# Kernel tuning notes

Hardware: AMD Instinct MI355X
Metric: run time of the kernel (lower is better)

## Reference

```python
import jax, jax.numpy as jnp
import numpy as np

K = 5  # up_kernel

def bilinear(x, hw):
    # torch F.interpolate bilinear, align_corners=False (half-pixel), no antialias
    return jax.image.resize(x, x.shape[:2] + hw, method='linear', antialias=False)

def nearest2x(x):
    return jnp.repeat(jnp.repeat(x, 2, axis=2), 2, axis=3)

def conv3x3(x, w, b):
    y = jax.lax.conv_general_dilated(x, w, (1, 1), [(1, 1), (1, 1)],
                                     dimension_numbers=('NCHW', 'OIHW', 'NCHW'))
    return y + b[None, :, None, None]

def carafe(x, mask):
    # x: [N,C,H,W]; mask: [N,K*K,H,W] softmax-normalized. scale_factor=1, up_group=1.
    N, C, H, W = x.shape
    r = K // 2
    xp = jnp.pad(x, ((0, 0), (0, 0), (r, r), (r, r)))
    out = jnp.zeros_like(x)
    idx = 0
    for di in range(K):
        for dj in range(K):
            out = out + xp[:, :, di:di + H, dj:dj + W] * mask[:, idx:idx + 1]
            idx += 1
    return out

def setup_inputs() -> dict:
    key = jax.random.key(0)
    ks = jax.random.split(key, 6)
    feat = jax.random.normal(ks[0], (1, 32, 96, 96), jnp.float32)
    seg = jax.random.normal(ks[1], (1, 19, 96, 96), jnp.float32)
    img = jax.random.uniform(ks[2], (1, 3, 384, 384), jnp.float32)
    w_enc0 = jax.random.normal(ks[3], (25, 35, 3, 3), jnp.float32) * 0.05
    b_enc0 = jnp.zeros((25,), jnp.float32)
    w_enc1 = jax.random.normal(ks[4], (25, 35, 3, 3), jnp.float32) * 0.05
    b_enc1 = jnp.zeros((25,), jnp.float32)
    return {'feat': feat, 'seg': seg, 'img': img,
            'w_enc0': w_enc0, 'b_enc0': b_enc0, 'w_enc1': w_enc1, 'b_enc1': b_enc1}

def reference(feat, seg, img, w_enc0, b_enc0, w_enc1, b_enc1):
    weights = [(w_enc0, b_enc0), (w_enc1, b_enc1)]
    for i in range(2):
        Hf, Wf = feat.shape[-2], feat.shape[-1]
        resized_img = bilinear(img, (2 * Hf, 2 * Wf))
        # high-boost filtering: img_hf = img - lowpass(img) + img
        lr = bilinear(resized_img, (Hf, Wf))
        lr = bilinear(lr, (2 * Hf, 2 * Wf))
        img_hf = 2.0 * resized_img - lr
        feat_up = nearest2x(feat)
        seg_up = nearest2x(seg)
        w, b = weights[i]
        mask = conv3x3(jnp.concatenate([feat_up, img_hf], axis=1), w, b)
        # kernel_normalizer: pixel_shuffle(1)=identity, softmax over the 25 kernel taps
        mask = jax.nn.softmax(mask, axis=1)
        seg = carafe(seg_up, mask)
        feat = carafe(feat_up, mask)
    return seg
```

## Files before the change

kernel.cpp:

```cpp
#include <hip/hip_runtime.h>


#define TPB 256

__global__ __launch_bounds__(TPB) void repack_kernel(
    const float* __restrict__ w, float* __restrict__ W2, float* __restrict__ wTh) {
  int i = blockIdx.x * TPB + threadIdx.x;
  if (i < 12800) {
    int oc = i % 25; int j = i / 25;
    int src = j & 3; j >>= 2;
    int ic = j & 31; int p = j >> 5;
    int py = p >> 1, px = p & 1;
    int a = src >> 1, b = src & 1;
    float s = 0.f;
    for (int ky = 0; ky < 3; ++ky) {
      int rs = (py == 0) ? (ky >= 1) : (ky >= 2);
      if (rs != a) continue;
      for (int kx = 0; kx < 3; ++kx) {
        int cs = (px == 0) ? (kx >= 1) : (kx >= 2);
        if (cs != b) continue;
        s += w[oc * 315 + ic * 9 + ky * 3 + kx];
      }
    }
    W2[i] = s;
  } else if (i < 12800 + 675) {
    int k = i - 12800;
    int oc = k % 25; int j = k / 25;
    int h = j % 3; int tap = j / 3;
    wTh[k] = w[oc * 315 + (32 + h) * 9 + tap];
  }
}

__global__ __launch_bounds__(TPB) void down2_kernel(
    const float* __restrict__ in, float* __restrict__ out, int C, int H, int W) {
  int idx = blockIdx.x * blockDim.x + threadIdx.x;
  int N = C * H * W;
  if (idx >= N) return;
  int x = idx % W; int t = idx / W; int y = t % H; int c = t / H;
  const float* p = in + ((c * 2 * H) + 2 * y) * (2 * W) + 2 * x;
  out[idx] = 0.25f * (p[0] + p[1] + p[2 * W] + p[2 * W + 1]);
}

__global__ __launch_bounds__(TPB) void highboost_kernel(
    const float* __restrict__ base, const float* __restrict__ lr,
    float* __restrict__ out, int C, int H, int W) {
  const int OH = 2 * H, OW = 2 * W;
  int idx = blockIdx.x * blockDim.x + threadIdx.x;
  int N = C * OH * OW;
  if (idx >= N) return;
  int x = idx % OW; int t = idx / OW; int y = t % OH; int c = t / OH;
  int m = y >> 1; int ya, yb; float wya, wyb;
  if ((y & 1) == 0) { ya = (m - 1 < 0) ? 0 : m - 1; yb = m; wya = 0.25f; wyb = 0.75f; }
  else             { ya = m; yb = (m + 1 >= H) ? H - 1 : m + 1; wya = 0.75f; wyb = 0.25f; }
  int n = x >> 1; int xa, xb; float wxa, wxb;
  if ((x & 1) == 0) { xa = (n - 1 < 0) ? 0 : n - 1; xb = n; wxa = 0.25f; wxb = 0.75f; }
  else             { xa = n; xb = (n + 1 >= W) ? W - 1 : n + 1; wxa = 0.75f; wxb = 0.25f; }
  const float* p = lr + c * H * W;
  float up = wya * (wxa * p[ya * W + xa] + wxb * p[ya * W + xb])
           + wyb * (wxa * p[yb * W + xa] + wxb * p[yb * W + xb]);
  out[idx] = 2.0f * base[idx] - up;
}

__global__ __launch_bounds__(512, 4) void conv_softmax_kernel(
    const float* __restrict__ feat, const float* __restrict__ hf,
    const float* __restrict__ W2, const float* __restrict__ wTh,
    const float* __restrict__ b, float* __restrict__ mask,
    int Hf, int Wf) {
  const int OH = 2 * Hf, OW = 2 * Wf, Np = OH * OW, fplane = Hf * Wf;
  __shared__ float red[8][64][26];

  const int t = threadIdx.x;
  const int lane = t & 63;
  const int s = __builtin_amdgcn_readfirstlane(t >> 6);
  const int par = blockIdx.x & 3;
  const int bt = blockIdx.x >> 2;
  const int TW = Wf >> 5;
  const int gx0 = (bt % TW) << 5;
  const int gy0 = (bt / TW) << 1;
  const int py = par >> 1, px = par & 1;
  const int gy = gy0 + (lane >> 5);
  const int gx = gx0 + (lane & 31);

  int r0 = gy - 1 + py; const bool zr0 = (r0 < 0);      if (zr0) r0 = 0;
  int r1 = gy + py;     const bool zr1 = (r1 >= Hf);    if (zr1) r1 = Hf - 1;
  int c0 = gx - 1 + px; const bool zc0 = (c0 < 0);      if (zc0) c0 = 0;
  int c1 = gx + px;     const bool zc1 = (c1 >= Wf);    if (zc1) c1 = Wf - 1;
  const int o00 = r0 * Wf + c0, o01 = r0 * Wf + c1;
  const int o10 = r1 * Wf + c0, o11 = r1 * Wf + c1;

  float acc[25];
#pragma unroll
  for (int oc = 0; oc < 25; ++oc) acc[oc] = 0.f;

  const int fbeg_tab[8] = {0, 3, 6, 9, 14, 19, 24, 28};
  const int fend_tab[8] = {3, 6, 9, 14, 19, 24, 28, 32};
  const int fbeg = fbeg_tab[s], fend = fend_tab[s];

  for (int ic = fbeg; ic < fend; ++ic) {
    const float* fp = feat + ic * fplane;
    float v00 = (zr0 | zc0) ? 0.f : fp[o00];
    float v01 = (zr0 | zc1) ? 0.f : fp[o01];
    float v10 = (zr1 | zc0) ? 0.f : fp[o10];
    float v11 = (zr1 | zc1) ? 0.f : fp[o11];
    const float* wp = W2 + (size_t)((par * 32 + ic) * 4) * 25;
#pragma unroll
    for (int oc = 0; oc < 25; ++oc)
      acc[oc] += v00 * wp[oc] + v01 * wp[25 + oc] + v10 * wp[50 + oc] + v11 * wp[75 + oc];
  }

  if (s < 3) {
    const int x = 2 * gx + px, y = 2 * gy + py;
    const float* hp = hf + s * Np;
#pragma unroll
    for (int ky = 0; ky < 3; ++ky) {
      int yy = y + ky - 1;
      bool vy = (yy >= 0) && (yy < OH);
      int yo = (vy ? yy : 0) * OW;
#pragma unroll
      for (int kx = 0; kx < 3; ++kx) {
        int xx = x + kx - 1;
        bool vv = vy && (xx >= 0) && (xx < OW);
        float v = vv ? hp[yo + (vv ? xx : 0)] : 0.f;
        const float* wp = wTh + ((ky * 3 + kx) * 3 + s) * 25;
#pragma unroll
        for (int oc = 0; oc < 25; ++oc) acc[oc] = fmaf(v, wp[oc], acc[oc]);
      }
    }
  }

#pragma unroll
  for (int oc = 0; oc < 25; ++oc) red[s][lane][oc] = acc[oc];
  __syncthreads();
  for (int i = t; i < 1600; i += 512) {
    int oc = i % 25, p2 = i / 25;
    float sum = red[0][p2][oc];
#pragma unroll
    for (int k = 1; k < 8; ++k) sum += red[k][p2][oc];
    red[0][p2][oc] = sum + b[oc];
  }
  __syncthreads();
  if (t < 64) {
    float mx = red[0][t][0];
#pragma unroll
    for (int oc = 1; oc < 25; ++oc) mx = fmaxf(mx, red[0][t][oc]);
    float ssum = 0.f;
#pragma unroll
    for (int oc = 0; oc < 25; ++oc) {
      float e = __expf(red[0][t][oc] - mx); red[0][t][oc] = e; ssum += e;
    }
    float inv = 1.0f / ssum;
#pragma unroll
    for (int oc = 0; oc < 25; ++oc) red[0][t][oc] *= inv;
  }
  __syncthreads();
  {
    const int p2 = t & 63;
    const int gy2 = gy0 + (p2 >> 5), gx2 = gx0 + (p2 & 31);
    const int pix = (2 * gy2 + py) * OW + (2 * gx2 + px);
    for (int oc = s; oc < 25; oc += 8)
      mask[oc * Np + pix] = red[0][p2][oc];
  }
}

__device__ __forceinline__ void carafe_apply(
    const float* __restrict__ in, float* __restrict__ out, int C,
    int fplane, int Np, int pix, const float cw[9],
    const int sy[3], const int sx[3], int Wf) {
  for (int c = 0; c < C; ++c) {
    const float* p = in + c * fplane;
    const float* r0 = p + sy[0] * Wf;
    const float* r1 = p + sy[1] * Wf;
    const float* r2 = p + sy[2] * Wf;
    float acc = cw[0] * r0[sx[0]] + cw[1] * r0[sx[1]] + cw[2] * r0[sx[2]]
              + cw[3] * r1[sx[0]] + cw[4] * r1[sx[1]] + cw[5] * r1[sx[2]]
              + cw[6] * r2[sx[0]] + cw[7] * r2[sx[1]] + cw[8] * r2[sx[2]];
    out[c * Np + pix] = acc;
  }
}

__global__ __launch_bounds__(TPB) void carafe_kernel(
    const float* __restrict__ mask,
    const float* __restrict__ in0, float* __restrict__ out0, int C0,
    const float* __restrict__ in1, float* __restrict__ out1, int C1,
    int Hf, int Wf) {
  const int OH = 2 * Hf, OW = 2 * Wf;
  const int Np = OH * OW;
  int pix = blockIdx.x * blockDim.x + threadIdx.x;
  if (pix >= Np) return;
  int x = pix % OW, y = pix / OW;

  float cw[9];
#pragma unroll
  for (int i = 0; i < 9; ++i) cw[i] = 0.f;
  int ry0 = (y - 2) >> 1, rx0 = (x - 2) >> 1;
#pragma unroll
  for (int di = 0; di < 5; ++di) {
    int yy = y + di - 2;
    if (yy < 0 || yy >= OH) continue;
#pragma unroll
    for (int dj = 0; dj < 5; ++dj) {
      int xx = x + dj - 2;
      if (xx < 0 || xx >= OW) continue;
      int rx = (xx >> 1) - rx0;
      cw[((yy >> 1) - ry0) * 3 + rx] += mask[(di * 5 + dj) * Np + pix];
    }
  }
  int sy[3], sx[3];
#pragma unroll
  for (int i = 0; i < 3; ++i) {
    int v = ry0 + i; sy[i] = v < 0 ? 0 : (v >= Hf ? Hf - 1 : v);
    int u = rx0 + i; sx[i] = u < 0 ? 0 : (u >= Wf ? Wf - 1 : u);
  }
  const int fplane = Hf * Wf;
  carafe_apply(in0, out0, C0, fplane, Np, pix, cw, sy, sx, Wf);
  if (in1 != nullptr) carafe_apply(in1, out1, C1, fplane, Np, pix, cw, sy, sx, Wf);
}

extern "C" void kernel_launch(void* const* d_in, const int* in_sizes, int n_in,
                              void* d_out, int out_size, void* d_ws, size_t ws_size,
                              hipStream_t stream) {
  (void)in_sizes; (void)n_in; (void)out_size; (void)ws_size;
  const float* feat = (const float*)d_in[0];
  const float* seg  = (const float*)d_in[1];
  const float* img  = (const float*)d_in[2];
  const float* w0   = (const float*)d_in[3];
  const float* b0   = (const float*)d_in[4];
  const float* w1   = (const float*)d_in[5];
  const float* b1   = (const float*)d_in[6];
  float* out = (float*)d_out;

  float* ws   = (float*)d_ws;
  float* I192 = ws;
  float* I96  = I192 + 3 * 192 * 192;
  float* HF   = I96  + 3 * 96 * 96;
  float* MASK = HF   + 3 * 384 * 384;
  float* F1   = MASK + 25 * 384 * 384;
  float* S1   = F1   + 32 * 192 * 192;
  float* W2_0 = S1   + 19 * 192 * 192;
  float* WTH0 = W2_0 + 12800;
  float* W2_1 = WTH0 + 675;
  float* WTH1 = W2_1 + 12800;

  repack_kernel<<<53, TPB, 0, stream>>>(w0, W2_0, WTH0);
  repack_kernel<<<53, TPB, 0, stream>>>(w1, W2_1, WTH1);
  down2_kernel<<<1728, 64, 0, stream>>>(img, I192, 3, 192, 192);
  down2_kernel<<<432, 64, 0, stream>>>(I192, I96, 3, 96, 96);

  highboost_kernel<<<1728, 64, 0, stream>>>(I192, I96, HF, 3, 96, 96);
  conv_softmax_kernel<<<4 * 48 * 3, 512, 0, stream>>>(
      feat, HF, W2_0, WTH0, b0, MASK, 96, 96);
  carafe_kernel<<<576, 64, 0, stream>>>(
      MASK, seg, S1, 19, feat, F1, 32, 96, 96);

  highboost_kernel<<<6912, 64, 0, stream>>>(img, I192, HF, 3, 192, 192);
  conv_softmax_kernel<<<4 * 96 * 6, 512, 0, stream>>>(
      F1, HF, W2_1, WTH1, b1, MASK, 192, 192);
  carafe_kernel<<<2304, 64, 0, stream>>>(
      MASK, S1, out, 19, nullptr, nullptr, 0, 192, 192);
}
```

Before: 178.1 us.

## Collapse mask to 9 source-pixel weights in conv, merge launches, split carafe channels

The conv+softmax kernel now reduces the 25 softmax taps to the 9 source-pixel weights, using the 2x nearest structure and boundary validity. It writes 9 planes instead of 25, which cuts mask write and read traffic, and the carafe kernel just loads the 9 weights. The two repack launches are merged, the second downsample is fused into a new hf0 kernel, and block sizes go from 64 to 256. Carafe work is also split across channel groups with a 2D grid, and the feature-channel partition in conv is rebalanced. The cost is more specialised, hardcoded-size kernels and redundant recompute of the 96x96 image in hf0.

```diff
diff --git a/kernel.cpp b/kernel.cpp
--- a/kernel.cpp
+++ b/kernel.cpp
@@ -1,13 +1,16 @@
 #include <hip/hip_runtime.h>
 
 
-#define TPB 256
-
-__global__ __launch_bounds__(TPB) void repack_kernel(
-    const float* __restrict__ w, float* __restrict__ W2, float* __restrict__ wTh) {
-  int i = blockIdx.x * TPB + threadIdx.x;
-  if (i < 12800) {
-    int oc = i % 25; int j = i / 25;
+__global__ __launch_bounds__(256) void repack_kernel(
+    const float* __restrict__ w0s, const float* __restrict__ w1s,
+    float* __restrict__ W2a, float* __restrict__ wTha,
+    float* __restrict__ W2b, float* __restrict__ wThb) {
+  int i = blockIdx.x * 256 + threadIdx.x;
+  const float* w; float* W2; float* wTh; int k = i;
+  if (i < 13475) { w = w0s; W2 = W2a; wTh = wTha; }
+  else { k = i - 13475; if (k >= 13475) return; w = w1s; W2 = W2b; wTh = wThb; }
+  if (k < 12800) {
+    int oc = k % 25; int j = k / 25;
     int src = j & 3; j >>= 2;
     int ic = j & 31; int p = j >> 5;
     int py = p >> 1, px = p & 1;
@@ -22,49 +25,68 @@
         s += w[oc * 315 + ic * 9 + ky * 3 + kx];
       }
     }
-    W2[i] = s;
-  } else if (i < 12800 + 675) {
-    int k = i - 12800;
-    int oc = k % 25; int j = k / 25;
+    W2[k] = s;
+  } else {
+    int kk = k - 12800;
+    int oc = kk % 25; int j = kk / 25;
     int h = j % 3; int tap = j / 3;
-    wTh[k] = w[oc * 315 + (32 + h) * 9 + tap];
-  }
-}
-
-__global__ __launch_bounds__(TPB) void down2_kernel(
-    const float* __restrict__ in, float* __restrict__ out, int C, int H, int W) {
-  int idx = blockIdx.x * blockDim.x + threadIdx.x;
-  int N = C * H * W;
-  if (idx >= N) return;
-  int x = idx % W; int t = idx / W; int y = t % H; int c = t / H;
-  const float* p = in + ((c * 2 * H) + 2 * y) * (2 * W) + 2 * x;
-  out[idx] = 0.25f * (p[0] + p[1] + p[2 * W] + p[2 * W + 1]);
-}
-
-__global__ __launch_bounds__(TPB) void highboost_kernel(
+    wTh[kk] = w[oc * 315 + (32 + h) * 9 + tap];
+  }
+}
+
+__global__ __launch_bounds__(256) void down2_kernel(
+    const float* __restrict__ in, float* __restrict__ out) {
+  int idx = blockIdx.x * 256 + threadIdx.x;
+  if (idx >= 3 * 192 * 192) return;
+  int x = idx % 192; int t = idx / 192; int y = t % 192; int c = t / 192;
+  const float* p = in + (c * 384 + 2 * y) * 384 + 2 * x;
+  out[idx] = 0.25f * (p[0] + p[1] + p[384] + p[385]);
+}
+
+__global__ __launch_bounds__(256) void hf0_kernel(
+    const float* __restrict__ I192, float* __restrict__ out) {
+  int idx = blockIdx.x * 256 + threadIdx.x;
+  if (idx >= 3 * 192 * 192) return;
+  int x = idx % 192; int t = idx / 192; int y = t % 192; int c = t / 192;
+  int m = y >> 1; int ya, yb; float wya, wyb;
+  if ((y & 1) == 0) { ya = m - 1 < 0 ? 0 : m - 1; yb = m; wya = 0.25f; wyb = 0.75f; }
+  else             { ya = m; yb = m + 1 > 95 ? 95 : m + 1; wya = 0.75f; wyb = 0.25f; }
+  int n = x >> 1; int xa, xb; float wxa, wxb;
+  if ((x & 1) == 0) { xa = n - 1 < 0 ? 0 : n - 1; xb = n; wxa = 0.25f; wxb = 0.75f; }
+  else             { xa = n; xb = n + 1 > 95 ? 95 : n + 1; wxa = 0.75f; wxb = 0.25f; }
+  const float* base = I192 + c * 192 * 192;
+  auto I96v = [&](int mm, int nn) {
+    const float* p = base + (2 * mm) * 192 + 2 * nn;
+    return 0.25f * (p[0] + p[1] + p[192] + p[193]);
+  };
+  float up = wya * (wxa * I96v(ya, xa) + wxb * I96v(ya, xb))
+           + wyb * (wxa * I96v(yb, xa) + wxb * I96v(yb, xb));
+  out[idx] = 2.0f * base[y * 192 + x] - up;
+}
+
+__global__ __launch_bounds__(256) void highboost_kernel(
     const float* __restrict__ base, const float* __restrict__ lr,
-    float* __restrict__ out, int C, int H, int W) {
-  const int OH = 2 * H, OW = 2 * W;
-  int idx = blockIdx.x * blockDim.x + threadIdx.x;
-  int N = C * OH * OW;
-  if (idx >= N) return;
-  int x = idx % OW; int t = idx / OW; int y = t % OH; int c = t / OH;
+    float* __restrict__ out) {
+  const int H = 192, OW = 384;
+  int idx = blockIdx.x * 256 + threadIdx.x;
+  if (idx >= 3 * 384 * 384) return;
+  int x = idx % OW; int t = idx / OW; int y = t % 384; int c = t / 384;
   int m = y >> 1; int ya, yb; float wya, wyb;
-  if ((y & 1) == 0) { ya = (m - 1 < 0) ? 0 : m - 1; yb = m; wya = 0.25f; wyb = 0.75f; }
-  else             { ya = m; yb = (m + 1 >= H) ? H - 1 : m + 1; wya = 0.75f; wyb = 0.25f; }
+  if ((y & 1) == 0) { ya = m - 1 < 0 ? 0 : m - 1; yb = m; wya = 0.25f; wyb = 0.75f; }
+  else             { ya = m; yb = m + 1 >= H ? H - 1 : m + 1; wya = 0.75f; wyb = 0.25f; }
   int n = x >> 1; int xa, xb; float wxa, wxb;
-  if ((x & 1) == 0) { xa = (n - 1 < 0) ? 0 : n - 1; xb = n; wxa = 0.25f; wxb = 0.75f; }
-  else             { xa = n; xb = (n + 1 >= W) ? W - 1 : n + 1; wxa = 0.75f; wxb = 0.25f; }
-  const float* p = lr + c * H * W;
-  float up = wya * (wxa * p[ya * W + xa] + wxb * p[ya * W + xb])
-           + wyb * (wxa * p[yb * W + xa] + wxb * p[yb * W + xb]);
+  if ((x & 1) == 0) { xa = n - 1 < 0 ? 0 : n - 1; xb = n; wxa = 0.25f; wxb = 0.75f; }
+  else             { xa = n; xb = n + 1 >= H ? H - 1 : n + 1; wxa = 0.75f; wxb = 0.25f; }
+  const float* p = lr + c * H * H;
+  float up = wya * (wxa * p[ya * H + xa] + wxb * p[ya * H + xb])
+           + wyb * (wxa * p[yb * H + xa] + wxb * p[yb * H + xb]);
   out[idx] = 2.0f * base[idx] - up;
 }
 
 __global__ __launch_bounds__(512, 4) void conv_softmax_kernel(
     const float* __restrict__ feat, const float* __restrict__ hf,
     const float* __restrict__ W2, const float* __restrict__ wTh,
-    const float* __restrict__ b, float* __restrict__ mask,
+    const float* __restrict__ b, float* __restrict__ CW,
     int Hf, int Wf) {
   const int OH = 2 * Hf, OW = 2 * Wf, Np = OH * OW, fplane = Hf * Wf;
   __shared__ float red[8][64][26];
@@ -92,9 +114,10 @@
 #pragma unroll
   for (int oc = 0; oc < 25; ++oc) acc[oc] = 0.f;
 
-  const int fbeg_tab[8] = {0, 3, 6, 9, 14, 19, 24, 28};
-  const int fend_tab[8] = {3, 6, 9, 14, 19, 24, 28, 32};
-  const int fbeg = fbeg_tab[s], fend = fend_tab[s];
+  const int fbeg = s == 0 ? 0 : s == 1 ? 2 : s == 2 ? 4 : s == 3 ? 6
+                 : s == 4 ? 12 : s == 5 ? 17 : s == 6 ? 22 : 27;
+  const int fend = s == 0 ? 2 : s == 1 ? 4 : s == 2 ? 6 : s == 3 ? 12
+                 : s == 4 ? 17 : s == 5 ? 22 : s == 6 ? 27 : 32;
 
   for (int ic = fbeg; ic < fend; ++ic) {
     const float* fp = feat + ic * fplane;
@@ -139,81 +162,103 @@
     red[0][p2][oc] = sum + b[oc];
   }
   __syncthreads();
+
   if (t < 64) {
-    float mx = red[0][t][0];
-#pragma unroll
-    for (int oc = 1; oc < 25; ++oc) mx = fmaxf(mx, red[0][t][oc]);
+    const int gy2 = gy0 + (t >> 5), gx2 = gx0 + (t & 31);
+    const int y = 2 * gy2 + py, x = 2 * gx2 + px;
+    float m[25];
+#pragma unroll
+    for (int oc = 0; oc < 25; ++oc) m[oc] = red[0][t][oc];
+    float mx = m[0];
+#pragma unroll
+    for (int oc = 1; oc < 25; ++oc) mx = fmaxf(mx, m[oc]);
     float ssum = 0.f;
 #pragma unroll
-    for (int oc = 0; oc < 25; ++oc) {
-      float e = __expf(red[0][t][oc] - mx); red[0][t][oc] = e; ssum += e;
-    }
+    for (int oc = 0; oc < 25; ++oc) { m[oc] = __expf(m[oc] - mx); ssum += m[oc]; }
     float inv = 1.0f / ssum;
-#pragma unroll
-    for (int oc = 0; oc < 25; ++oc) red[0][t][oc] *= inv;
-  }
-  __syncthreads();
-  {
-    const int p2 = t & 63;
-    const int gy2 = gy0 + (p2 >> 5), gx2 = gx0 + (p2 & 31);
-    const int pix = (2 * gy2 + py) * OW + (2 * gx2 + px);
-    for (int oc = s; oc < 25; oc += 8)
-      mask[oc * Np + pix] = red[0][p2][oc];
-  }
-}
-
-__device__ __forceinline__ void carafe_apply(
-    const float* __restrict__ in, float* __restrict__ out, int C,
-    int fplane, int Np, int pix, const float cw[9],
-    const int sy[3], const int sx[3], int Wf) {
-  for (int c = 0; c < C; ++c) {
-    const float* p = in + c * fplane;
+
+    bool vy[5], vx[5];
+#pragma unroll
+    for (int d = 0; d < 5; ++d) {
+      vy[d] = (unsigned)(y + d - 2) < (unsigned)OH;
+      vx[d] = (unsigned)(x + d - 2) < (unsigned)OW;
+    }
+    float rs[3][5];
+    if (py == 0) {
+#pragma unroll
+      for (int dj = 0; dj < 5; ++dj) {
+        float m0 = (vy[0] && vx[dj]) ? m[0 + dj] : 0.f;
+        float m1 = (vy[1] && vx[dj]) ? m[5 + dj] : 0.f;
+        float m2 = (vy[2] && vx[dj]) ? m[10 + dj] : 0.f;
+        float m3 = (vy[3] && vx[dj]) ? m[15 + dj] : 0.f;
+        float m4 = (vy[4] && vx[dj]) ? m[20 + dj] : 0.f;
+        rs[0][dj] = m0 + m1; rs[1][dj] = m2 + m3; rs[2][dj] = m4;
+      }
+    } else {
+#pragma unroll
+      for (int dj = 0; dj < 5; ++dj) {
+        float m0 = (vy[0] && vx[dj]) ? m[0 + dj] : 0.f;
+        float m1 = (vy[1] && vx[dj]) ? m[5 + dj] : 0.f;
+        float m2 = (vy[2] && vx[dj]) ? m[10 + dj] : 0.f;
+        float m3 = (vy[3] && vx[dj]) ? m[15 + dj] : 0.f;
+        float m4 = (vy[4] && vx[dj]) ? m[20 + dj] : 0.f;
+        rs[0][dj] = m0; rs[1][dj] = m1 + m2; rs[2][dj] = m3 + m4;
+      }
+    }
+    float cw[9];
+#pragma unroll
+    for (int r = 0; r < 3; ++r) {
+      if (px == 0) {
+        cw[r * 3 + 0] = rs[r][0] + rs[r][1];
+        cw[r * 3 + 1] = rs[r][2] + rs[r][3];
+        cw[r * 3 + 2] = rs[r][4];
+      } else {
+        cw[r * 3 + 0] = rs[r][0];
+        cw[r * 3 + 1] = rs[r][1] + rs[r][2];
+        cw[r * 3 + 2] = rs[r][3] + rs[r][4];
+      }
+    }
+    const int pix = y * OW + x;
+#pragma unroll
+    for (int tap = 0; tap < 9; ++tap) CW[tap * Np + pix] = cw[tap] * inv;
+  }
+}
+
+__global__ __launch_bounds__(256) void carafe_kernel(
+    const float* __restrict__ CW,
+    const float* __restrict__ in0, float* __restrict__ out0, int C0,
+    const float* __restrict__ in1, float* __restrict__ out1, int C1,
+    int CS, int Hf, int Wf) {
+  const int OW = 2 * Wf;
+  const int Np = 4 * Hf * Wf;
+  int pix = blockIdx.x * 256 + threadIdx.x;
+  if (pix >= Np) return;
+  int x = pix % OW, y = pix / OW;
+  int ry0 = (y >> 1) - 1, rx0 = (x >> 1) - 1;
+  int sy[3], sx[3];
+#pragma unroll
+  for (int i = 0; i < 3; ++i) {
+    int v = ry0 + i; sy[i] = v < 0 ? 0 : (v >= Hf ? Hf - 1 : v);
+    int u = rx0 + i; sx[i] = u < 0 ? 0 : (u >= Wf ? Wf - 1 : u);
+  }
+  float cw[9];
+#pragma unroll
+  for (int i = 0; i < 9; ++i) cw[i] = CW[i * Np + pix];
+  const int fplane = Hf * Wf;
+  int cbeg = blockIdx.y * CS;
+  int cend = cbeg + CS; int Ct = C0 + C1; if (cend > Ct) cend = Ct;
+  for (int c = cbeg; c < cend; ++c) {
+    const float* p; float* q;
+    if (c < C0) { p = in0 + c * fplane; q = out0 + c * Np; }
+    else        { p = in1 + (c - C0) * fplane; q = out1 + (c - C0) * Np; }
     const float* r0 = p + sy[0] * Wf;
     const float* r1 = p + sy[1] * Wf;
     const float* r2 = p + sy[2] * Wf;
     float acc = cw[0] * r0[sx[0]] + cw[1] * r0[sx[1]] + cw[2] * r0[sx[2]]
               + cw[3] * r1[sx[0]] + cw[4] * r1[sx[1]] + cw[5] * r1[sx[2]]
               + cw[6] * r2[sx[0]] + cw[7] * r2[sx[1]] + cw[8] * r2[sx[2]];
-    out[c * Np + pix] = acc;
-  }
-}
-
-__global__ __launch_bounds__(TPB) void carafe_kernel(
-    const float* __restrict__ mask,
-    const float* __restrict__ in0, float* __restrict__ out0, int C0,
-    const float* __restrict__ in1, float* __restrict__ out1, int C1,
-    int Hf, int Wf) {
-  const int OH = 2 * Hf, OW = 2 * Wf;
-  const int Np = OH * OW;
-  int pix = blockIdx.x * blockDim.x + threadIdx.x;
-  if (pix >= Np) return;
-  int x = pix % OW, y = pix / OW;
-
-  float cw[9];
-#pragma unroll
-  for (int i = 0; i < 9; ++i) cw[i] = 0.f;
-  int ry0 = (y - 2) >> 1, rx0 = (x - 2) >> 1;
-#pragma unroll
-  for (int di = 0; di < 5; ++di) {
-    int yy = y + di - 2;
-    if (yy < 0 || yy >= OH) continue;
-#pragma unroll
-    for (int dj = 0; dj < 5; ++dj) {
-      int xx = x + dj - 2;
-      if (xx < 0 || xx >= OW) continue;
-      int rx = (xx >> 1) - rx0;
-      cw[((yy >> 1) - ry0) * 3 + rx] += mask[(di * 5 + dj) * Np + pix];
-    }
-  }
-  int sy[3], sx[3];
-#pragma unroll
-  for (int i = 0; i < 3; ++i) {
-    int v = ry0 + i; sy[i] = v < 0 ? 0 : (v >= Hf ? Hf - 1 : v);
-    int u = rx0 + i; sx[i] = u < 0 ? 0 : (u >= Wf ? Wf - 1 : u);
-  }
-  const int fplane = Hf * Wf;
-  carafe_apply(in0, out0, C0, fplane, Np, pix, cw, sy, sx, Wf);
-  if (in1 != nullptr) carafe_apply(in1, out1, C1, fplane, Np, pix, cw, sy, sx, Wf);
+    q[pix] = acc;
+  }
 }
 
 extern "C" void kernel_launch(void* const* d_in, const int* in_sizes, int n_in,
@@ -231,30 +276,27 @@
 
   float* ws   = (float*)d_ws;
   float* I192 = ws;
-  float* I96  = I192 + 3 * 192 * 192;
-  float* HF   = I96  + 3 * 96 * 96;
-  float* MASK = HF   + 3 * 384 * 384;
-  float* F1   = MASK + 25 * 384 * 384;
+  float* HF   = I192 + 3 * 192 * 192;
+  float* CWb  = HF   + 3 * 384 * 384;
+  float* F1   = CWb  + 9 * 384 * 384;
   float* S1   = F1   + 32 * 192 * 192;
   float* W2_0 = S1   + 19 * 192 * 192;
   float* WTH0 = W2_0 + 12800;
   float* W2_1 = WTH0 + 675;
   float* WTH1 = W2_1 + 12800;
 
-  repack_kernel<<<53, TPB, 0, stream>>>(w0, W2_0, WTH0);
-  repack_kernel<<<53, TPB, 0, stream>>>(w1, W2_1, WTH1);
-  down2_kernel<<<1728, 64, 0, stream>>>(img, I192, 3, 192, 192);
-  down2_kernel<<<432, 64, 0, stream>>>(I192, I96, 3, 96, 96);
-
-  highboost_kernel<<<1728, 64, 0, stream>>>(I192, I96, HF, 3, 96, 96);
+  repack_kernel<<<106, 256, 0, stream>>>(w0, w1, W2_0, WTH0, W2_1, WTH1);
+  down2_kernel<<<432, 256, 0, stream>>>(img, I192);
+
+  hf0_kernel<<<432, 256, 0, stream>>>(I192, HF);
   conv_softmax_kernel<<<4 * 48 * 3, 512, 0, stream>>>(
-      feat, HF, W2_0, WTH0, b0, MASK, 96, 96);
-  carafe_kernel<<<576, 64, 0, stream>>>(
-      MASK, seg, S1, 19, feat, F1, 32, 96, 96);
-
-  highboost_kernel<<<6912, 64, 0, stream>>>(img, I192, HF, 3, 192, 192);
+      feat, HF, W2_0, WTH0, b0, CWb, 96, 96);
+  carafe_kernel<<<dim3(144, 3), 256, 0, stream>>>(
+      CWb, seg, S1, 19, feat, F1, 32, 17, 96, 96);
+
+  highboost_kernel<<<1728, 256, 0, stream>>>(img, I192, HF);
   conv_softmax_kernel<<<4 * 96 * 6, 512, 0, stream>>>(
-      F1, HF, W2_1, WTH1, b1, MASK, 192, 192);
-  carafe_kernel<<<2304, 64, 0, stream>>>(
-      MASK, S1, out, 19, nullptr, nullptr, 0, 192, 192);
-}
+      F1, HF, W2_1, WTH1, b1, CWb, 192, 192);
+  carafe_kernel<<<dim3(576, 2), 256, 0, stream>>>(
+      CWb, S1, out, 19, nullptr, nullptr, 0, 10, 192, 192);
+}
```

Result: no change. 175.6 us (-1.4%).
